# Kernel tuning notes

Hardware: AMD Instinct MI355X
Metric: run time of the kernel (lower is better)

The kernel has to match this reference:

```python
import jax, jax.numpy as jnp
import numpy as np

B, D = 64, 1024
ETA = 0.01  # learning_rate

def setup_inputs() -> dict:
    key = jax.random.key(0)
    k1, k2, k3 = jax.random.split(key, 3)
    W = jax.random.normal(k1, (B, D, D), dtype=jnp.float32) * 0.02
    x = jax.random.normal(k2, (B, D, 1), dtype=jnp.float32)
    grad_L = jax.random.normal(k3, (B, D, 1), dtype=jnp.float32)
    return {"W": W, "x": x, "grad_L": grad_L}

def reference(W, x, grad_L):
    # W_{t+1} = W (I - x x^T) - eta * grad_L x^T
    # Algebraically identical O(d^2) form: W - (W x) x^T - eta * grad_L x^T
    Wx = jnp.einsum('bij,bjo->bio', W, x)            # [B, D, 1]
    update = jnp.einsum('bio,bjo->bij', Wx + ETA * grad_L, x)  # (Wx + eta*gL) x^T
    return W - update
```

## Files before the change

### kernel.cpp

```cpp
#include <hip/hip_runtime.h>


#define ETA 0.01f

__global__ __launch_bounds__(256) void internal_opt_kernel(
    const float* __restrict__ W,
    const float* __restrict__ x,
    const float* __restrict__ gL,
    float* __restrict__ out)
{
    const int row = blockIdx.x;
    const int b   = row >> 10;
    const int t   = threadIdx.x;

    const long long woff = (long long)row * 1024 + (t << 2);
    const float4 w4 = *(const float4*)(W + woff);
    const float4 x4 = *(const float4*)(x + (long long)(b << 10) + (t << 2));

    float p = w4.x * x4.x + w4.y * x4.y + w4.z * x4.z + w4.w * x4.w;

    #pragma unroll
    for (int off = 32; off > 0; off >>= 1)
        p += __shfl_down(p, off, 64);

    __shared__ float wave_sum[4];
    __shared__ float s_bcast;
    const int wave = t >> 6;
    if ((t & 63) == 0) wave_sum[wave] = p;
    __syncthreads();
    if (t == 0) {
        const float Wx = wave_sum[0] + wave_sum[1] + wave_sum[2] + wave_sum[3];
        s_bcast = Wx + ETA * gL[row];
    }
    __syncthreads();
    const float s = s_bcast;

    float4 o4;
    o4.x = w4.x - s * x4.x;
    o4.y = w4.y - s * x4.y;
    o4.z = w4.z - s * x4.z;
    o4.w = w4.w - s * x4.w;
    *(float4*)(out + woff) = o4;
}

extern "C" void kernel_launch(void* const* d_in, const int* in_sizes, int n_in,
                              void* d_out, int out_size, void* d_ws, size_t ws_size,
                              hipStream_t stream)
{
    const float* W  = (const float*)d_in[0];
    const float* x  = (const float*)d_in[1];
    const float* gL = (const float*)d_in[2];
    float* out = (float*)d_out;

    const int B = 64, D = 1024;
    dim3 grid(B * D);
    dim3 block(256);
    internal_opt_kernel<<<grid, block, 0, stream>>>(W, x, gL, out);
}
```

Before: 414.0 us.

## Assign four rows per wavefront with register-held W and no block barriers

Each 64-lane wavefront now handles four full rows. It loads all of W for those rows plus the shared x vector into registers, reduces each dot product with xor shuffles, and writes the rank-1 update directly. This removes the per-row block of 256 threads, the shared-memory reduction and both __syncthreads, and it raises memory-level parallelism per thread. The cost is higher register use per lane, which may reduce occupancy, and the grid shrinks by a factor of 16.

```diff
diff --git a/kernel.cpp b/kernel.cpp
--- a/kernel.cpp
+++ b/kernel.cpp
@@ -9,38 +9,62 @@
     const float* __restrict__ gL,
     float* __restrict__ out)
 {
-    const int row = blockIdx.x;
-    const int b   = row >> 10;
-    const int t   = threadIdx.x;
+    const int lane = threadIdx.x & 63;
+    const int wid  = (blockIdx.x << 2) + (threadIdx.x >> 6);
+    const int row0 = wid << 2;
+    const int b    = row0 >> 10;
 
-    const long long woff = (long long)row * 1024 + (t << 2);
-    const float4 w4 = *(const float4*)(W + woff);
-    const float4 x4 = *(const float4*)(x + (long long)(b << 10) + (t << 2));
+    float g[4];
+    #pragma unroll
+    for (int r = 0; r < 4; ++r) g[r] = gL[row0 + r];
 
-    float p = w4.x * x4.x + w4.y * x4.y + w4.z * x4.z + w4.w * x4.w;
+    const float* xb = x + (b << 10);
+    float4 xf[4];
+    #pragma unroll
+    for (int k = 0; k < 4; ++k)
+        xf[k] = *(const float4*)(xb + ((lane + (k << 6)) << 2));
+
+    float4 w[4][4];
+    #pragma unroll
+    for (int r = 0; r < 4; ++r) {
+        const float* Wr = W + ((long long)(row0 + r) << 10);
+        #pragma unroll
+        for (int k = 0; k < 4; ++k)
+            w[r][k] = *(const float4*)(Wr + ((lane + (k << 6)) << 2));
+    }
+
+    float p[4];
+    #pragma unroll
+    for (int r = 0; r < 4; ++r) {
+        float a = 0.f;
+        #pragma unroll
+        for (int k = 0; k < 4; ++k)
+            a += w[r][k].x * xf[k].x + w[r][k].y * xf[k].y
+               + w[r][k].z * xf[k].z + w[r][k].w * xf[k].w;
+        p[r] = a;
+    }
 
     #pragma unroll
-    for (int off = 32; off > 0; off >>= 1)
-        p += __shfl_down(p, off, 64);
+    for (int off = 32; off > 0; off >>= 1) {
+        #pragma unroll
+        for (int r = 0; r < 4; ++r)
+            p[r] += __shfl_xor(p[r], off, 64);
+    }
 
-    __shared__ float wave_sum[4];
-    __shared__ float s_bcast;
-    const int wave = t >> 6;
-    if ((t & 63) == 0) wave_sum[wave] = p;
-    __syncthreads();
-    if (t == 0) {
-        const float Wx = wave_sum[0] + wave_sum[1] + wave_sum[2] + wave_sum[3];
-        s_bcast = Wx + ETA * gL[row];
+    #pragma unroll
+    for (int r = 0; r < 4; ++r) {
+        const float s = p[r] + ETA * g[r];
+        float* Or = out + ((long long)(row0 + r) << 10);
+        #pragma unroll
+        for (int k = 0; k < 4; ++k) {
+            float4 o;
+            o.x = w[r][k].x - s * xf[k].x;
+            o.y = w[r][k].y - s * xf[k].y;
+            o.z = w[r][k].z - s * xf[k].z;
+            o.w = w[r][k].w - s * xf[k].w;
+            *(float4*)(Or + ((lane + (k << 6)) << 2)) = o;
+        }
     }
-    __syncthreads();
-    const float s = s_bcast;
-
-    float4 o4;
-    o4.x = w4.x - s * x4.x;
-    o4.y = w4.y - s * x4.y;
-    o4.z = w4.z - s * x4.z;
-    o4.w = w4.w - s * x4.w;
-    *(float4*)(out + woff) = o4;
 }
 
 extern "C" void kernel_launch(void* const* d_in, const int* in_sizes, int n_in,
@@ -53,7 +77,7 @@
     float* out = (float*)d_out;
 
     const int B = 64, D = 1024;
-    dim3 grid(B * D);
+    dim3 grid((B * D) / 16);
     dim3 block(256);
     internal_opt_kernel<<<grid, block, 0, stream>>>(W, x, gL, out);
 }
```

After: 433.6 us. 1.05x slower.
